# Kernel tuning notes

Measured on AMD Instinct MI355X. Metric: run time of the kernel, lower is better.

The kernel has to match this reference:

```python
import jax, jax.numpy as jnp
import numpy as np

N_NODES = 50000
N_EDGES = 800000
EPS = 1e-5

def _xavier(key, shape):
    fan_in, fan_out = shape[1], shape[0]
    lim = float(np.sqrt(6.0 / (fan_in + fan_out)))
    return jax.random.uniform(key, shape, jnp.float32, -lim, lim)

def setup_inputs() -> dict:
    key = jax.random.key(0)
    ks = jax.random.split(key, 12)
    x = jax.random.normal(ks[0], (N_NODES, 166), jnp.float32)
    edge_index = jax.random.randint(ks[1], (2, N_EDGES), 0, N_NODES, jnp.int32)
    dims = [(256, 166), (128, 256), (64, 128)]
    inp = {"x": x, "edge_index": edge_index}
    # SAGEConv layers: lin_l (applied to aggregated neighbors, has bias) and lin_r (self)
    names = ["1", "2", "e"]
    for i, (nm, (do, di)) in enumerate(zip(names, dims)):
        inp[f"Wl{nm}"] = _xavier(ks[2 + 2 * i], (do, di))
        inp[f"Wr{nm}"] = _xavier(ks[3 + 2 * i], (do, di))
        inp[f"b{nm}"] = jnp.zeros((do,), jnp.float32)
    # BatchNorm params for the two hidden conv layers
    inp["g1"] = jnp.ones((256,), jnp.float32); inp["bt1"] = jnp.zeros((256,), jnp.float32)
    inp["g2"] = jnp.ones((128,), jnp.float32); inp["bt2"] = jnp.zeros((128,), jnp.float32)
    # classifier
    inp["Wc"] = _xavier(ks[8], (2, 64))
    inp["bc"] = jnp.zeros((2,), jnp.float32)
    return inp

def _sage_conv(x, src, dst, Wl, Wr, b):
    # mean aggregation of source features at destination nodes
    agg = jax.ops.segment_sum(x[src], dst, num_segments=N_NODES)  # [N, d]
    deg = jax.ops.segment_sum(jnp.ones((src.shape[0],), x.dtype), dst, num_segments=N_NODES)
    agg = agg / jnp.maximum(deg, 1.0)[:, None]
    return agg @ Wl.T + x @ Wr.T + b

def _bn(x, g, b):
    m = jnp.mean(x, axis=0)
    v = jnp.var(x, axis=0)
    return (x - m) * jax.lax.rsqrt(v + EPS) * g + b

def reference(x, edge_index, Wl1, Wr1, b1, Wl2, Wr2, b2, Wle, Wre, be, g1, bt1, g2, bt2, Wc, bc):
    src, dst = edge_index[0], edge_index[1]
    h = _sage_conv(x, src, dst, Wl1, Wr1, b1)
    h = jax.nn.relu(_bn(h, g1, bt1))
    h = _sage_conv(h, src, dst, Wl2, Wr2, b2)
    h = jax.nn.relu(_bn(h, g2, bt2))
    embeddings = _sage_conv(h, src, dst, Wle, Wre, be)  # [N, 64]
    logits = embeddings @ Wc.T + bc  # [N, 2]
    return (logits, embeddings)
```

## Files before the change

kernel.cpp:

```cpp
#include <hip/hip_runtime.h>

#define NN 50000
#define NE 800000
#define NB 256
#define BNODES ((NN + NB - 1) / NB)
#define CAP 4096
#define BPART_BLKS ((NE + 8191) / 8192)
#define PREP_BLKS ((NN * 112 + 255) / 256)
#define PACK_BLKS ((180224 + 255) / 256)
static constexpr float BN_EPS = 1e-5f;

typedef __attribute__((ext_vector_type(8))) short bf16x8;
typedef __attribute__((ext_vector_type(4))) float f32x4;

__device__ inline unsigned short f2bf(float f) {
  unsigned int u = __float_as_uint(f);
  return (unsigned short)((u + 0x7FFFu + ((u >> 16) & 1u)) >> 16);
}
__device__ inline float bf2f(unsigned int h) { return __uint_as_float(h << 16); }
__device__ inline void gl_lds16(const char* g, char* l) {
  __builtin_amdgcn_global_load_lds((const __attribute__((address_space(1))) void*)g,
                                   (__attribute__((address_space(3))) void*)l, 16, 0, 0);
}

__device__ void dev_bpart(int bb, const int* __restrict__ src, const int* __restrict__ dst,
                          int* __restrict__ bcur, uint2* __restrict__ pairs) {
  __shared__ int cnt[NB], lbase[NB], lcur[NB];
  int t = threadIdx.x;
  cnt[t] = 0;
  __syncthreads();
  int e0 = bb * 8192 + t;
#pragma unroll
  for (int i = 0; i < 32; ++i) {
    int e = e0 + i * 256;
    if (e < NE) atomicAdd(&cnt[dst[e] / BNODES], 1);
  }
  __syncthreads();
  lbase[t] = cnt[t] ? (t * CAP + atomicAdd(&bcur[t], cnt[t])) : 0;
  lcur[t] = 0;
  __syncthreads();
#pragma unroll
  for (int i = 0; i < 32; ++i) {
    int e = e0 + i * 256;
    if (e < NE) {
      int d = dst[e];
      int b = d / BNODES;
      int p = atomicAdd(&lcur[b], 1);
      pairs[(size_t)lbase[b] + p] = uint2{(unsigned)src[e], (unsigned)d};
    }
  }
}

__global__ void k_front(const int* __restrict__ src, const int* __restrict__ dst,
                        int* __restrict__ bcur, uint2* __restrict__ pairs,
                        const float* __restrict__ x, unsigned int* __restrict__ xbu,
                        unsigned int* __restrict__ aggX,
                        const float* __restrict__ Wl1, const float* __restrict__ Wr1,
                        const float* __restrict__ Wl2, const float* __restrict__ Wr2,
                        const float* __restrict__ Wle, const float* __restrict__ Wre,
                        unsigned short* __restrict__ w1c, unsigned short* __restrict__ w2s,
                        unsigned short* __restrict__ w3s,
                        float* __restrict__ bnacc) {
  int b = blockIdx.x;
  if (b < BPART_BLKS) {
    dev_bpart(b, src, dst, bcur, pairs);
    return;
  }
  b -= BPART_BLKS;
  if (b < PREP_BLKS) {
    int i = b * 256 + threadIdx.x;
    if (i >= NN * 112) return;
    int r = i / 112, q = i - r * 112;
    if (q < 84) {
      int c0 = 2 * q, c1 = c0 + 1;
      float v0 = (c0 < 166) ? x[(size_t)r * 166 + c0] : 0.f;
      float v1 = (c1 < 166) ? x[(size_t)r * 166 + c1] : 0.f;
      xbu[(size_t)r * 96 + q] = (unsigned)f2bf(v0) | ((unsigned)f2bf(v1) << 16);
    } else if (q < 96) {
      xbu[(size_t)r * 96 + q] = 0u;
    } else if (q < 109) {
      aggX[(size_t)r * 96 + 83 + (q - 96)] = 0u;
    }
    return;
  }
  b -= PREP_BLKS;
  if (b < PACK_BLKS) {
    int idx = b * 256 + threadIdx.x;
    if (idx < 98304) {
      int n = idx / 384, k = idx - n * 384;
      float v = 0.f;
      if (k < 166) v = Wl1[(size_t)n * 166 + k];
      else if (k >= 192 && k < 358) v = Wr1[(size_t)n * 166 + (k - 192)];
      w1c[idx] = f2bf(v);
    } else if (idx < 163840) {
      int j = idx - 98304;
      int n = j / 256, k = j - n * 256;
      w2s[j] = f2bf(n < 128 ? Wl2[(size_t)n * 256 + k] : Wr2[(size_t)(n - 128) * 256 + k]);
    } else if (idx < 180224) {
      int j = idx - 163840;
      int n = j / 128, k = j - n * 128;
      w3s[j] = f2bf(n < 64 ? Wle[(size_t)n * 128 + k] : Wre[(size_t)(n - 64) * 128 + k]);
    }
    return;
  }
  int z = (b - PACK_BLKS) * 256 + threadIdx.x;
  if (z < 1024) bnacc[z] = 0.f;
}

__global__ void k_bscatter(const uint2* __restrict__ pairs, const int* __restrict__ bcur,
                           int2* __restrict__ begend, int* __restrict__ col) {
  __shared__ int dcnt[NB], ts[NB], doff[NB], dcur[NB];
  int t = threadIdx.x;
  int b = blockIdx.x;
  int n0 = b * BNODES;
  int ncnt = min(NN - n0, BNODES);
  int e0 = b * CAP, e1 = e0 + bcur[b];
  dcnt[t] = 0;
  __syncthreads();
  for (int e = e0 + t; e < e1; e += 256) atomicAdd(&dcnt[pairs[e].y - n0], 1);
  __syncthreads();
  ts[t] = dcnt[t];
  __syncthreads();
#pragma unroll
  for (int off = 1; off < NB; off <<= 1) {
    int u = (t >= off) ? ts[t - off] : 0;
    __syncthreads();
    ts[t] += u;
    __syncthreads();
  }
  doff[t] = ts[t] - dcnt[t];
  dcur[t] = 0;
  if (t < ncnt) begend[n0 + t] = int2{e0 + doff[t], e0 + doff[t] + dcnt[t]};
  __syncthreads();
  for (int e = e0 + t; e < e1; e += 256) {
    uint2 pr = pairs[e];
    int ld = pr.y - n0;
    int p = atomicAdd(&dcur[ld], 1);
    col[e0 + doff[ld] + p] = (int)pr.x;
  }
}

template <int D, int U, bool FUSE, bool OUTBF, bool CLS>
__global__ __launch_bounds__(256) void k_aggb(
    const unsigned int* __restrict__ feat, int fsu,
    const int2* __restrict__ begend, const int* __restrict__ col,
    const unsigned int* __restrict__ self, int ssu,
    const float* __restrict__ bias,
    void* __restrict__ outv, int osu,
    const float* __restrict__ Wc, const float* __restrict__ bc,
    float* __restrict__ logits) {
  constexpr int D2 = D / 2;
  constexpr int LPN = (D2 < 64) ? D2 : 64;
  constexpr int NPB = 256 / LPN;
  constexpr int C = (D2 + LPN - 1) / LPN;
  int node = blockIdx.x * NPB + threadIdx.x / LPN;
  if (node >= NN) return;
  int lane = threadIdx.x % LPN;
  int2 be = begend[node];
  int beg = be.x, end = be.y;
  float ax[C], ay[C];
#pragma unroll
  for (int c = 0; c < C; ++c) { ax[c] = 0.f; ay[c] = 0.f; }

  int j = beg;
  for (; j + U <= end; j += U) {
    const unsigned int* fp[U];
#pragma unroll
    for (int u = 0; u < U; ++u) fp[u] = feat + (size_t)col[j + u] * fsu;
#pragma unroll
    for (int c = 0; c < C; ++c) {
      int p = lane + c * LPN;
      unsigned int t[U];
#pragma unroll
      for (int u = 0; u < U; ++u) t[u] = (p < D2) ? fp[u][p] : 0u;
#pragma unroll
      for (int u = 0; u < U; ++u) {
        ax[c] += bf2f(t[u] & 0xffffu);
        ay[c] += bf2f(t[u] >> 16);
      }
    }
  }
  for (; j < end; ++j) {
    const unsigned int* fr = feat + (size_t)col[j] * fsu;
#pragma unroll
    for (int c = 0; c < C; ++c) {
      int p = lane + c * LPN;
      if (p < D2) {
        unsigned int t = fr[p];
        ax[c] += bf2f(t & 0xffffu);
        ay[c] += bf2f(t >> 16);
      }
    }
  }
  float inv = 1.0f / fmaxf((float)(end - beg), 1.0f);
  float s0 = 0.f, s1 = 0.f;
#pragma unroll
  for (int c = 0; c < C; ++c) {
    int p = lane + c * LPN;
    if (p < D2) {
      float vx = ax[c] * inv, vy = ay[c] * inv;
      if constexpr (FUSE) {
        unsigned int s = self[(size_t)node * ssu + p];
        vx += bf2f(s & 0xffffu) + bias[2 * p];
        vy += bf2f(s >> 16) + bias[2 * p + 1];
      }
      if constexpr (OUTBF) {
        unsigned int o = (unsigned int)f2bf(vx) | ((unsigned int)f2bf(vy) << 16);
        ((unsigned int*)outv)[(size_t)node * osu + p] = o;
      } else {
        float2 o{vx, vy};
        *reinterpret_cast<float2*>((float*)outv + (size_t)node * osu + 2 * p) = o;
      }
      if constexpr (CLS) {
        s0 += vx * Wc[2 * p] + vy * Wc[2 * p + 1];
        s1 += vx * Wc[64 + 2 * p] + vy * Wc[64 + 2 * p + 1];
      }
    }
  }
  if constexpr (CLS) {
#pragma unroll
    for (int m = 1; m < LPN; m <<= 1) {
      s0 += __shfl_xor(s0, m);
      s1 += __shfl_xor(s1, m);
    }
    if (lane == 0) {
      logits[node * 2 + 0] = s0 + bc[0];
      logits[node * 2 + 1] = s1 + bc[1];
    }
  }
}

template <bool BIASED, bool STATS>
__global__ __launch_bounds__(256) void k_gemm_mfma(
    const unsigned short* __restrict__ A0, const unsigned short* __restrict__ A1,
    int K1, int Astride, int KC,
    const unsigned short* __restrict__ W,
    const float* __restrict__ bias,
    unsigned short* __restrict__ out, int Ntot,
    float* __restrict__ statacc) {
  __shared__ __align__(16) char lds[65536];
  int tid = threadIdx.x;
  int lane = tid & 63;
  int w = tid >> 6;
  int wr = w >> 1, wc = w & 1;
  int m0 = blockIdx.x * 128;
  int n0 = blockIdx.y * 128;

  int srow = lane >> 3;
  int scol = (lane & 7) << 4;
  int ssw = scol ^ (srow << 4);
  const char* Wb = (const char*)W;

  f32x4 acc[4][4];
#pragma unroll
  for (int i = 0; i < 4; ++i)
#pragma unroll
    for (int j = 0; j < 4; ++j) acc[i][j] = f32x4{0.f, 0.f, 0.f, 0.f};

  auto stage = [&](int buf, int k0) {
    const char* Ab = (const char*)(k0 < K1 ? A0 : A1);
    int koff = k0 < K1 ? k0 : k0 - K1;
    char* dst = lds + buf * 32768 + w * 4096;
#pragma unroll
    for (int i = 0; i < 4; ++i) {
      int row = w * 32 + i * 8 + srow;
      int ga = m0 + row;
      ga = ga < NN ? ga : NN - 1;
      gl_lds16(Ab + ((size_t)ga * Astride + koff) * 2 + ssw, dst + i * 1024);
      gl_lds16(Wb + ((size_t)(n0 + row) * KC + k0) * 2 + ssw, dst + 16384 + i * 1024);
    }
  };
  auto compute = [&](int buf) {
    char* lA = lds + buf * 32768;
    char* lB = lA + 16384;
#pragma unroll
    for (int ks = 0; ks < 2; ++ks) {
      bf16x8 af[4], bfr[4];
      int ac = ks * 64 + ((lane >> 4) << 4);
#pragma unroll
      for (int f = 0; f < 4; ++f) {
        int ar = wr * 64 + f * 16 + (lane & 15);
        af[f] = *reinterpret_cast<const bf16x8*>(lA + ar * 128 + (ac ^ ((ar & 7) << 4)));
        int br = wc * 64 + f * 16 + (lane & 15);
        bfr[f] = *reinterpret_cast<const bf16x8*>(lB + br * 128 + (ac ^ ((br & 7) << 4)));
      }
#pragma unroll
      for (int fm = 0; fm < 4; ++fm)
#pragma unroll
        for (int fn = 0; fn < 4; ++fn)
          acc[fm][fn] = __builtin_amdgcn_mfma_f32_16x16x32_bf16(af[fm], bfr[fn], acc[fm][fn], 0, 0, 0);
    }
  };

  int nt = KC >> 6;
  stage(0, 0);
  if (nt > 1) stage(1, 64);
  for (int t = 0; t < nt - 1; ++t) {
    asm volatile("s_waitcnt vmcnt(8)" ::: "memory");
    __builtin_amdgcn_s_barrier();
    compute(t & 1);
    __builtin_amdgcn_s_barrier();
    if (t + 2 < nt) stage(t & 1, (t + 2) << 6);
  }
  asm volatile("s_waitcnt vmcnt(0)" ::: "memory");
  __builtin_amdgcn_s_barrier();
  compute((nt - 1) & 1);

  int nbase = n0 + wc * 64 + (lane & 15);
  float bv[4] = {0.f, 0.f, 0.f, 0.f};
  if constexpr (BIASED) {
#pragma unroll
    for (int fn = 0; fn < 4; ++fn) bv[fn] = bias[nbase + fn * 16];
  }
  float ssum[4] = {0.f, 0.f, 0.f, 0.f}, sqs[4] = {0.f, 0.f, 0.f, 0.f};
#pragma unroll
  for (int fm = 0; fm < 4; ++fm) {
    int mbase = m0 + wr * 64 + fm * 16 + ((lane >> 4) << 2);
#pragma unroll
    for (int j = 0; j < 4; ++j) {
      int m = mbase + j;
      if (m < NN) {
#pragma unroll
        for (int fn = 0; fn < 4; ++fn) {
          float v = acc[fm][fn][j] + bv[fn];
          out[(size_t)m * Ntot + nbase + fn * 16] = f2bf(v);
          if constexpr (STATS) { ssum[fn] += v; sqs[fn] += v * v; }
        }
      }
    }
  }
  if constexpr (STATS) {
#pragma unroll
    for (int fn = 0; fn < 4; ++fn) {
      float s = ssum[fn], q = sqs[fn];
      s += __shfl_xor(s, 16); s += __shfl_xor(s, 32);
      q += __shfl_xor(q, 16); q += __shfl_xor(q, 32);
      if (lane < 16) {
        atomicAdd(&statacc[nbase + fn * 16], s);
        atomicAdd(&statacc[Ntot + nbase + fn * 16], q);
      }
    }
  }
}

template <int N, bool BF>
__global__ __launch_bounds__(256) void k_bn_stats2(const void* __restrict__ hv,
                                                   float* __restrict__ acc) {
  constexpr int CP = N / 2;
  constexpr int RG = 256 / CP;
  int cp = threadIdx.x % CP, rg = threadIdx.x / CP;
  int rpb = (NN + gridDim.x - 1) / gridDim.x;
  int r0 = blockIdx.x * rpb, r1 = min(r0 + rpb, NN);
  float s0 = 0.f, s1 = 0.f, q0 = 0.f, q1 = 0.f;
  for (int r = r0 + rg; r < r1; r += RG) {
    float v0, v1;
    if constexpr (BF) {
      unsigned int u = ((const unsigned int*)hv)[(size_t)r * CP + cp];
      v0 = bf2f(u & 0xffffu); v1 = bf2f(u >> 16);
    } else {
      float2 u = ((const float2*)hv)[(size_t)r * CP + cp];
      v0 = u.x; v1 = u.y;
    }
    s0 += v0; s1 += v1; q0 += v0 * v0; q1 += v1 * v1;
  }
  __shared__ float l0[256], l1[256], l2[256], l3[256];
  l0[threadIdx.x] = s0; l1[threadIdx.x] = s1; l2[threadIdx.x] = q0; l3[threadIdx.x] = q1;
  __syncthreads();
  if (rg == 0) {
#pragma unroll
    for (int g = 1; g < RG; ++g) {
      s0 += l0[g * CP + cp]; s1 += l1[g * CP + cp];
      q0 += l2[g * CP + cp]; q1 += l3[g * CP + cp];
    }
    atomicAdd(&acc[2 * cp], s0);
    atomicAdd(&acc[2 * cp + 1], s1);
    atomicAdd(&acc[N + 2 * cp], q0);
    atomicAdd(&acc[N + 2 * cp + 1], q1);
  }
}

template <int N, bool INF32>
__global__ void k_bn_apply2(const void* __restrict__ hv, const float* __restrict__ acc,
                            const float* __restrict__ g, const float* __restrict__ b,
                            unsigned int* __restrict__ out) {
  constexpr int N2 = N / 2;
  int p = blockIdx.x * 256 + threadIdx.x;
  if (p >= NN * N2) return;
  int cp = p % N2;
  int c0 = 2 * cp, c1 = c0 + 1;
  float v0, v1;
  if constexpr (INF32) {
    float2 u = reinterpret_cast<const float2*>(hv)[p];
    v0 = u.x; v1 = u.y;
  } else {
    unsigned int u = reinterpret_cast<const unsigned int*>(hv)[p];
    v0 = bf2f(u & 0xffffu); v1 = bf2f(u >> 16);
  }
  float m0 = acc[c0] * (1.0f / NN);
  float m1 = acc[c1] * (1.0f / NN);
  float sc0 = g[c0] * rsqrtf(acc[N + c0] * (1.0f / NN) - m0 * m0 + BN_EPS);
  float sc1 = g[c1] * rsqrtf(acc[N + c1] * (1.0f / NN) - m1 * m1 + BN_EPS);
  float r0 = fmaxf((v0 - m0) * sc0 + b[c0], 0.f);
  float r1 = fmaxf((v1 - m1) * sc1 + b[c1], 0.f);
  out[p] = (unsigned int)f2bf(r0) | ((unsigned int)f2bf(r1) << 16);
}

extern "C" void kernel_launch(void* const* d_in, const int* in_sizes, int n_in,
                              void* d_out, int out_size, void* d_ws, size_t ws_size,
                              hipStream_t stream) {
  const float* x   = (const float*)d_in[0];
  const int* ei    = (const int*)d_in[1];
  const float* Wl1 = (const float*)d_in[2];
  const float* Wr1 = (const float*)d_in[3];
  const float* b1  = (const float*)d_in[4];
  const float* Wl2 = (const float*)d_in[5];
  const float* Wr2 = (const float*)d_in[6];
  const float* b2  = (const float*)d_in[7];
  const float* Wle = (const float*)d_in[8];
  const float* Wre = (const float*)d_in[9];
  const float* be  = (const float*)d_in[10];
  const float* g1  = (const float*)d_in[11];
  const float* bt1 = (const float*)d_in[12];
  const float* g2  = (const float*)d_in[13];
  const float* bt2 = (const float*)d_in[14];
  const float* Wc  = (const float*)d_in[15];
  const float* bc  = (const float*)d_in[16];

  const int* src = ei;
  const int* dst = ei + NE;

  char* ws = (char*)d_ws;
  size_t off = 0;
  auto take = [&](size_t bytes) -> char* {
    char* p = ws + off;
    off = (off + bytes + 255) & ~(size_t)255;
    return p;
  };
  int* bkt_cur   = (int*)take(1024);
  float* bnacc1  = (float*)take(2048);
  float* bnacc2  = (float*)take(2048);
  int2* begend   = (int2*)take((size_t)NN * 8);
  uint2* pairs   = (uint2*)take((size_t)NB * CAP * 8);
  int* col       = (int*)take((size_t)NB * CAP * 4);
  unsigned short* w1c = (unsigned short*)take((size_t)256 * 384 * 2);
  unsigned short* w2s = (unsigned short*)take((size_t)256 * 256 * 2);
  unsigned short* w3s = (unsigned short*)take((size_t)128 * 128 * 2);
  unsigned int* xbu  = (unsigned int*)take((size_t)NN * 96 * 4);
  unsigned int* aggX = (unsigned int*)take((size_t)NN * 96 * 4);
  char* P1 = take((size_t)NN * 256 * 2);
  char* P0 = take((size_t)NN * 256 * 2);

  unsigned short* h1raw = (unsigned short*)P1;
  unsigned short* h1    = (unsigned short*)P0;
  unsigned short* z2    = (unsigned short*)P1;
  float*          h2raw = (float*)P0;
  unsigned short* h2    = (unsigned short*)P1;
  unsigned short* z3    = (unsigned short*)P0;

  float* logits = (float*)d_out;
  float* emb    = (float*)d_out + (size_t)NN * 2;

  hipMemsetAsync(bkt_cur, 0, 1024, stream);

  {
    int grid = BPART_BLKS + PREP_BLKS + PACK_BLKS + 4;
    k_front<<<grid, 256, 0, stream>>>(src, dst, bkt_cur, pairs, x, xbu, aggX,
                                      Wl1, Wr1, Wl2, Wr2, Wle, Wre, w1c, w2s, w3s, bnacc1);
  }
  k_bscatter<<<NB, NB, 0, stream>>>(pairs, bkt_cur, begend, col);

  k_aggb<166, 4, false, true, false><<<(NN + 3) / 4, 256, 0, stream>>>(
      xbu, 96, begend, col, nullptr, 0, nullptr, aggX, 96, nullptr, nullptr, nullptr);
  {
    dim3 g((NN + 127) / 128, 2);
    k_gemm_mfma<true, true><<<g, 256, 0, stream>>>(
        (const unsigned short*)aggX, (const unsigned short*)xbu, 192, 192, 384,
        w1c, b1, h1raw, 256, bnacc1);
  }
  k_bn_apply2<256, false><<<(NN * 128 + 255) / 256, 256, 0, stream>>>(
      h1raw, bnacc1, g1, bt1, (unsigned int*)h1);

  {
    dim3 g((NN + 127) / 128, 2);
    k_gemm_mfma<false, false><<<g, 256, 0, stream>>>(
        h1, h1, 1 << 30, 256, 256, w2s, nullptr, z2, 256, nullptr);
  }
  k_aggb<128, 8, true, false, false><<<(NN + 3) / 4, 256, 0, stream>>>(
      (const unsigned int*)z2, 128, begend, col, (const unsigned int*)z2 + 64, 128, b2,
      h2raw, 128, nullptr, nullptr, nullptr);
  k_bn_stats2<128, false><<<512, 256, 0, stream>>>(h2raw, bnacc2);
  k_bn_apply2<128, true><<<(NN * 64 + 255) / 256, 256, 0, stream>>>(
      h2raw, bnacc2, g2, bt2, (unsigned int*)h2);

  {
    dim3 g((NN + 127) / 128, 1);
    k_gemm_mfma<false, false><<<g, 256, 0, stream>>>(
        h2, h2, 1 << 30, 128, 128, w3s, nullptr, z3, 128, nullptr);
  }
  k_aggb<64, 8, true, false, true><<<(NN + 7) / 8, 256, 0, stream>>>(
      (const unsigned int*)z3, 64, begend, col, (const unsigned int*)z3 + 32, 64, be,
      emb, 64, Wc, bc, logits);
}
```

Baseline: 289.3 us.

## Fuse BatchNorm apply and ReLU into the A-tile load of the following GEMM

Replaces the standalone BN-apply kernels with a tiny per-channel scale/shift kernel plus a new MFMA GEMM that applies scale, shift and ReLU while staging the A operand into LDS. This removes a full read and write pass over the 50000x256 and 50000x128 activations. Layer-2 aggregation output is now stored as bf16 rather than fp32, which halves its traffic but lowers precision for the BN statistics. The A loads now go through registers instead of direct-to-LDS, so latency hiding in the GEMM may suffer.

Result: faster. 274.0 us, median of 2 (-5.3%).

```diff
diff --git a/kernel.cpp b/kernel.cpp
--- a/kernel.cpp
+++ b/kernel.cpp
@@ -343,6 +343,128 @@
   }
 }
 
+__global__ __launch_bounds__(256) void k_gemm_bn(
+    const unsigned short* __restrict__ A, const float* __restrict__ scsh,
+    const unsigned short* __restrict__ W,
+    unsigned short* __restrict__ out, int KC, int Ntot) {
+  __shared__ __align__(16) char lds[65536];
+  int tid = threadIdx.x;
+  int lane = tid & 63;
+  int w = tid >> 6;
+  int wr = w >> 1, wc = w & 1;
+  int m0 = blockIdx.x * 128;
+  int n0 = blockIdx.y * 128;
+
+  int srow = lane >> 3;
+  int cb = (lane & 7) << 4;
+  int ssw = cb ^ (srow << 4);
+  int kk0 = (lane & 7) << 3;
+  const char* Wb = (const char*)W;
+
+  f32x4 acc[4][4];
+#pragma unroll
+  for (int i = 0; i < 4; ++i)
+#pragma unroll
+    for (int j = 0; j < 4; ++j) acc[i][j] = f32x4{0.f, 0.f, 0.f, 0.f};
+
+  uint4 areg[4];
+  float4 sc[4];
+
+  auto loadA = [&](int k0) {
+    int kk = k0 + kk0;
+    const float4* sp = (const float4*)(scsh + 2 * kk);
+    sc[0] = sp[0]; sc[1] = sp[1]; sc[2] = sp[2]; sc[3] = sp[3];
+#pragma unroll
+    for (int i = 0; i < 4; ++i) {
+      int row = w * 32 + i * 8 + srow;
+      int ga = m0 + row;
+      ga = ga < NN ? ga : NN - 1;
+      areg[i] = *reinterpret_cast<const uint4*>(A + (size_t)ga * KC + kk);
+    }
+  };
+  auto writeA = [&](int buf) {
+    char* dstb = lds + buf * 32768;
+#pragma unroll
+    for (int i = 0; i < 4; ++i) {
+      int row = w * 32 + i * 8 + srow;
+      uint4 v = areg[i], o;
+      float a, b;
+      a = fmaxf(bf2f(v.x & 0xffffu) * sc[0].x + sc[0].y, 0.f);
+      b = fmaxf(bf2f(v.x >> 16)     * sc[0].z + sc[0].w, 0.f);
+      o.x = (unsigned)f2bf(a) | ((unsigned)f2bf(b) << 16);
+      a = fmaxf(bf2f(v.y & 0xffffu) * sc[1].x + sc[1].y, 0.f);
+      b = fmaxf(bf2f(v.y >> 16)     * sc[1].z + sc[1].w, 0.f);
+      o.y = (unsigned)f2bf(a) | ((unsigned)f2bf(b) << 16);
+      a = fmaxf(bf2f(v.z & 0xffffu) * sc[2].x + sc[2].y, 0.f);
+      b = fmaxf(bf2f(v.z >> 16)     * sc[2].z + sc[2].w, 0.f);
+      o.z = (unsigned)f2bf(a) | ((unsigned)f2bf(b) << 16);
+      a = fmaxf(bf2f(v.w & 0xffffu) * sc[3].x + sc[3].y, 0.f);
+      b = fmaxf(bf2f(v.w >> 16)     * sc[3].z + sc[3].w, 0.f);
+      o.w = (unsigned)f2bf(a) | ((unsigned)f2bf(b) << 16);
+      *reinterpret_cast<uint4*>(dstb + row * 128 + (cb ^ ((row & 7) << 4))) = o;
+    }
+  };
+  auto stageW = [&](int buf, int k0) {
+    char* dst = lds + buf * 32768 + 16384 + w * 4096;
+#pragma unroll
+    for (int i = 0; i < 4; ++i) {
+      int row = w * 32 + i * 8 + srow;
+      gl_lds16(Wb + ((size_t)(n0 + row) * KC + k0) * 2 + ssw, dst + i * 1024);
+    }
+  };
+  auto compute = [&](int buf) {
+    char* lA = lds + buf * 32768;
+    char* lB = lA + 16384;
+#pragma unroll
+    for (int ks = 0; ks < 2; ++ks) {
+      bf16x8 af[4], bfr[4];
+      int ac = ks * 64 + ((lane >> 4) << 4);
+#pragma unroll
+      for (int f = 0; f < 4; ++f) {
+        int ar = wr * 64 + f * 16 + (lane & 15);
+        af[f] = *reinterpret_cast<const bf16x8*>(lA + ar * 128 + (ac ^ ((ar & 7) << 4)));
+        int br = wc * 64 + f * 16 + (lane & 15);
+        bfr[f] = *reinterpret_cast<const bf16x8*>(lB + br * 128 + (ac ^ ((br & 7) << 4)));
+      }
+#pragma unroll
+      for (int fm = 0; fm < 4; ++fm)
+#pragma unroll
+        for (int fn = 0; fn < 4; ++fn)
+          acc[fm][fn] = __builtin_amdgcn_mfma_f32_16x16x32_bf16(af[fm], bfr[fn], acc[fm][fn], 0, 0, 0);
+    }
+  };
+
+  int nt = KC >> 6;
+  loadA(0);
+  stageW(0, 0);
+  writeA(0);
+  __syncthreads();
+  int cur = 0;
+  for (int t = 0; t < nt; ++t) {
+    if (t + 1 < nt) { loadA((t + 1) << 6); stageW(cur ^ 1, (t + 1) << 6); }
+    compute(cur);
+    __syncthreads();
+    if (t + 1 < nt) writeA(cur ^ 1);
+    __syncthreads();
+    cur ^= 1;
+  }
+
+  int nbase = n0 + wc * 64 + (lane & 15);
+#pragma unroll
+  for (int fm = 0; fm < 4; ++fm) {
+    int mbase = m0 + wr * 64 + fm * 16 + ((lane >> 4) << 2);
+#pragma unroll
+    for (int j = 0; j < 4; ++j) {
+      int m = mbase + j;
+      if (m < NN) {
+#pragma unroll
+        for (int fn = 0; fn < 4; ++fn)
+          out[(size_t)m * Ntot + nbase + fn * 16] = f2bf(acc[fm][fn][j]);
+      }
+    }
+  }
+}
+
 template <int N, bool BF>
 __global__ __launch_bounds__(256) void k_bn_stats2(const void* __restrict__ hv,
                                                    float* __restrict__ acc) {
@@ -379,30 +501,15 @@
   }
 }
 
-template <int N, bool INF32>
-__global__ void k_bn_apply2(const void* __restrict__ hv, const float* __restrict__ acc,
-                            const float* __restrict__ g, const float* __restrict__ b,
-                            unsigned int* __restrict__ out) {
-  constexpr int N2 = N / 2;
-  int p = blockIdx.x * 256 + threadIdx.x;
-  if (p >= NN * N2) return;
-  int cp = p % N2;
-  int c0 = 2 * cp, c1 = c0 + 1;
-  float v0, v1;
-  if constexpr (INF32) {
-    float2 u = reinterpret_cast<const float2*>(hv)[p];
-    v0 = u.x; v1 = u.y;
-  } else {
-    unsigned int u = reinterpret_cast<const unsigned int*>(hv)[p];
-    v0 = bf2f(u & 0xffffu); v1 = bf2f(u >> 16);
-  }
-  float m0 = acc[c0] * (1.0f / NN);
-  float m1 = acc[c1] * (1.0f / NN);
-  float sc0 = g[c0] * rsqrtf(acc[N + c0] * (1.0f / NN) - m0 * m0 + BN_EPS);
-  float sc1 = g[c1] * rsqrtf(acc[N + c1] * (1.0f / NN) - m1 * m1 + BN_EPS);
-  float r0 = fmaxf((v0 - m0) * sc0 + b[c0], 0.f);
-  float r1 = fmaxf((v1 - m1) * sc1 + b[c1], 0.f);
-  out[p] = (unsigned int)f2bf(r0) | ((unsigned int)f2bf(r1) << 16);
+template <int N>
+__global__ void k_scsh(const float* __restrict__ acc, const float* __restrict__ g,
+                       const float* __restrict__ b, float* __restrict__ scsh) {
+  int c = threadIdx.x;
+  float mean = acc[c] * (1.0f / NN);
+  float var = acc[N + c] * (1.0f / NN) - mean * mean;
+  float sc = g[c] * rsqrtf(var + BN_EPS);
+  scsh[2 * c] = sc;
+  scsh[2 * c + 1] = b[c] - mean * sc;
 }
 
 extern "C" void kernel_launch(void* const* d_in, const int* in_sizes, int n_in,
@@ -439,6 +546,8 @@
   int* bkt_cur   = (int*)take(1024);
   float* bnacc1  = (float*)take(2048);
   float* bnacc2  = (float*)take(2048);
+  float* scsh1   = (float*)take(512 * 4);
+  float* scsh2   = (float*)take(256 * 4);
   int2* begend   = (int2*)take((size_t)NN * 8);
   uint2* pairs   = (uint2*)take((size_t)NB * CAP * 8);
   int* col       = (int*)take((size_t)NB * CAP * 4);
@@ -451,10 +560,8 @@
   char* P0 = take((size_t)NN * 256 * 2);
 
   unsigned short* h1raw = (unsigned short*)P1;
-  unsigned short* h1    = (unsigned short*)P0;
-  unsigned short* z2    = (unsigned short*)P1;
-  float*          h2raw = (float*)P0;
-  unsigned short* h2    = (unsigned short*)P1;
+  unsigned short* z2    = (unsigned short*)P0;
+  unsigned short* h2raw = (unsigned short*)P1;
   unsigned short* z3    = (unsigned short*)P0;
 
   float* logits = (float*)d_out;
@@ -477,25 +584,21 @@
         (const unsigned short*)aggX, (const unsigned short*)xbu, 192, 192, 384,
         w1c, b1, h1raw, 256, bnacc1);
   }
-  k_bn_apply2<256, false><<<(NN * 128 + 255) / 256, 256, 0, stream>>>(
-      h1raw, bnacc1, g1, bt1, (unsigned int*)h1);
+  k_scsh<256><<<1, 256, 0, stream>>>(bnacc1, g1, bt1, scsh1);
 
   {
     dim3 g((NN + 127) / 128, 2);
-    k_gemm_mfma<false, false><<<g, 256, 0, stream>>>(
-        h1, h1, 1 << 30, 256, 256, w2s, nullptr, z2, 256, nullptr);
-  }
-  k_aggb<128, 8, true, false, false><<<(NN + 3) / 4, 256, 0, stream>>>(
+    k_gemm_bn<<<g, 256, 0, stream>>>(h1raw, scsh1, w2s, z2, 256, 256);
+  }
+  k_aggb<128, 8, true, true, false><<<(NN + 3) / 4, 256, 0, stream>>>(
       (const unsigned int*)z2, 128, begend, col, (const unsigned int*)z2 + 64, 128, b2,
-      h2raw, 128, nullptr, nullptr, nullptr);
-  k_bn_stats2<128, false><<<512, 256, 0, stream>>>(h2raw, bnacc2);
-  k_bn_apply2<128, true><<<(NN * 64 + 255) / 256, 256, 0, stream>>>(
-      h2raw, bnacc2, g2, bt2, (unsigned int*)h2);
+      h2raw, 64, nullptr, nullptr, nullptr);
+  k_bn_stats2<128, true><<<512, 256, 0, stream>>>(h2raw, bnacc2);
+  k_scsh<128><<<1, 128, 0, stream>>>(bnacc2, g2, bt2, scsh2);
 
   {
     dim3 g((NN + 127) / 128, 1);
-    k_gemm_mfma<false, false><<<g, 256, 0, stream>>>(
-        h2, h2, 1 << 30, 128, 128, w3s, nullptr, z3, 128, nullptr);
+    k_gemm_bn<<<g, 256, 0, stream>>>(h2raw, scsh2, w3s, z3, 128, 128);
   }
   k_aggb<64, 8, true, false, true><<<(NN + 7) / 8, 256, 0, stream>>>(
       (const unsigned int*)z3, 64, begend, col, (const unsigned int*)z3 + 32, 64, be,
```
